# Kernel tuning notes

Hardware: AMD Instinct MI355X
Metric: run time of the kernel (lower is better)

## Reference

```python
import jax, jax.numpy as jnp
import numpy as np

S, B, D, E, H, REQ = 2048, 4, 256, 256, 8, 16  # seq, batch, hidden_dim, embed(=hidden_size), heads, band half-width


def setup_inputs() -> dict:
    key = jax.random.key(0)
    ks = jax.random.split(key, 12)
    w = lambda k, shape: jax.random.normal(k, shape, jnp.float32) * 0.02
    return {
        "mod": jax.random.normal(ks[0], (S, B, D), jnp.float32),
        "mask": jnp.zeros((B, S), jnp.float32),  # unused in speaker=False branch (kept for fidelity)
        "Wq": w(ks[1], (E, D)), "bq": jnp.zeros((E,), jnp.float32),
        "Wk": w(ks[2], (E, D)), "bk": jnp.zeros((E,), jnp.float32),
        "Wv": w(ks[3], (E, D)), "bv": jnp.zeros((E,), jnp.float32),
        "Win": w(ks[4], (3 * E, E)), "bin_": jnp.zeros((3 * E,), jnp.float32),  # MHA in_proj
        "Wout": w(ks[5], (E, E)), "bout": jnp.zeros((E,), jnp.float32),         # MHA out_proj
        "Wfc": w(ks[6], (D, E)), "bfc": jnp.zeros((D,), jnp.float32),           # self.fc
        "gamma": jnp.ones((D,), jnp.float32), "beta": jnp.zeros((D,), jnp.float32),
        "req": REQ,
    }


def reference(mod, mask, Wq, bq, Wk, bk, Wv, bv, Win, bin_, Wout, bout, Wfc, bfc, gamma, beta, req):
    s, b, d = mod.shape
    e = Wq.shape[0]
    hd = e // H
    # fc_q/k/v (pre-projection) then MultiheadAttention's own in_proj
    q = mod @ Wq.T + bq                       # (s, b, e)
    k = mod @ Wk.T + bk
    v = mod @ Wv.T + bv
    q = q @ Win[:e].T + bin_[:e]
    k = k @ Win[e:2 * e].T + bin_[e:2 * e]
    v = v @ Win[2 * e:].T + bin_[2 * e:]
    split = lambda x: x.reshape(s, b, H, hd).transpose(1, 2, 0, 3)  # (b, H, s, hd)
    qh, kh, vh = split(q), split(k), split(v)
    scores = jnp.einsum('bhqd,bhkd->bhqk', qh, kh) / jnp.sqrt(jnp.float32(hd))
    idx = jnp.arange(s)
    allowed = jnp.abs(idx[:, None] - idx[None, :]) < req  # band: diag + offsets 1..req-1
    scores = jnp.where(allowed[None, None], scores, -jnp.inf)
    attn = jax.nn.softmax(scores, axis=-1)                # attn dropout = identity (eval)
    ctx = jnp.einsum('bhqk,bhkd->bhqd', attn, vh)
    ctx = ctx.transpose(2, 0, 1, 3).reshape(s, b, e)
    ctx = ctx @ Wout.T + bout
    y = ctx @ Wfc.T + bfc + mod                           # dropout(0.5) = identity (eval), residual
    mu = jnp.mean(y, axis=-1, keepdims=True)
    var = jnp.var(y, axis=-1, keepdims=True)
    return (y - mu) / jnp.sqrt(var + 1e-6) * gamma + beta
```

## Files before the change

### kernel.cpp

```cpp
#include <hip/hip_runtime.h>
#include <hip/hip_bf16.h>
#include <math.h>

#define SS 2048
#define BB 4
#define DD 256
#define EE 256
#define HH 8
#define HD 32
#define TT (SS*BB)

typedef unsigned short ushortt;
typedef __attribute__((ext_vector_type(8))) short short8;
typedef __attribute__((ext_vector_type(4))) float f32x4;

__device__ __forceinline__ float bfbits2f(ushortt u) {
    return __uint_as_float(((unsigned int)u) << 16);
}
__device__ __forceinline__ ushortt f2bf_bits(float f) {
    unsigned int u = __float_as_uint(f);
    unsigned int r = u + 0x7FFFu + ((u >> 16) & 1u);
    return (ushortt)(r >> 16);
}

__device__ __forceinline__ int robust_req(const void* p) {
    int i = *(const int*)p;
    if (i >= 1 && i <= SS) return i;
    float f = __int_as_float(i);
    if (f >= 1.f && f <= (float)SS) return (int)(f + 0.5f);
    float b = bfbits2f(*(const ushortt*)p);
    if (b >= 1.f && b <= (float)SS) return (int)(b + 0.5f);
    return 16;
}

__global__ __launch_bounds__(256)
void fuse_fold(const float* __restrict__ mod,
               const float* __restrict__ Win,
               const float* __restrict__ Wq, const float* __restrict__ Wk,
               const float* __restrict__ Wv,
               const float* __restrict__ bq, const float* __restrict__ bk,
               const float* __restrict__ bv, const float* __restrict__ bin_,
               const float* __restrict__ Wfc, const float* __restrict__ Wout,
               const float* __restrict__ bout, const float* __restrict__ bfc,
               ushortt* __restrict__ Weffb, float* __restrict__ beff,
               ushortt* __restrict__ W2b, float* __restrict__ b2,
               ushortt* __restrict__ modb) {
    __shared__ __align__(16) ushortt ALds[64][264];
    __shared__ __align__(16) ushortt BLds[64][264];
    const int t = threadIdx.x;

    {
        size_t base = (size_t)blockIdx.x * 2048 + (size_t)t * 8;
        float4 v0 = *(const float4*)(mod + base);
        float4 v1 = *(const float4*)(mod + base + 4);
        ushort4 o0, o1;
        o0.x = f2bf_bits(v0.x); o0.y = f2bf_bits(v0.y);
        o0.z = f2bf_bits(v0.z); o0.w = f2bf_bits(v0.w);
        o1.x = f2bf_bits(v1.x); o1.y = f2bf_bits(v1.y);
        o1.z = f2bf_bits(v1.z); o1.w = f2bf_bits(v1.w);
        *(ushort4*)(modb + base)     = o0;
        *(ushort4*)(modb + base + 4) = o1;
    }
    if (blockIdx.x >= 64) return;

    const int mat = blockIdx.x >> 4;
    const int mt  = (blockIdx.x >> 2) & 3;
    const int nt  = blockIdx.x & 3;
    const int m0  = mt * 64, n0 = nt * 64;

    const float* Asrc = (mat == 3) ? (Wfc + (size_t)m0 * EE)
                                   : (Win + ((size_t)mat * EE + m0) * EE);
    const float* Bsrc = (mat == 0) ? Wq : (mat == 1) ? Wk : (mat == 2) ? Wv : Wout;

#pragma unroll
    for (int i = 0; i < 16; ++i) {
        int slot = t + 256 * i;
        int row = slot >> 6, c4 = slot & 63;
        float4 v = *(const float4*)(Asrc + (size_t)row * EE + c4 * 4);
        ushort4 o;
        o.x = f2bf_bits(v.x); o.y = f2bf_bits(v.y);
        o.z = f2bf_bits(v.z); o.w = f2bf_bits(v.w);
        *(ushort4*)&ALds[row][c4 * 4] = o;
    }
#pragma unroll
    for (int i = 0; i < 16; ++i) {
        int slot = t + 256 * i;
        int k = slot >> 4, c4 = slot & 15;
        float4 v = *(const float4*)(Bsrc + (size_t)k * DD + n0 + c4 * 4);
        BLds[c4 * 4 + 0][k] = f2bf_bits(v.x);
        BLds[c4 * 4 + 1][k] = f2bf_bits(v.y);
        BLds[c4 * 4 + 2][k] = f2bf_bits(v.z);
        BLds[c4 * 4 + 3][k] = f2bf_bits(v.w);
    }
    if (nt == 0) {
        const float* bvec = (mat == 0) ? bq : (mat == 1) ? bk : (mat == 2) ? bv : bout;
        int r = t >> 2, qq = t & 3;
        const float* arow = Asrc + (size_t)r * EE + qq * 64;
        const float* bv64 = bvec + qq * 64;
        float p = 0.f;
#pragma unroll
        for (int j = 0; j < 64; ++j) p += arow[j] * bv64[j];
        p += __shfl_xor(p, 1);
        p += __shfl_xor(p, 2);
        if (qq == 0) {
            if (mat == 3) b2[m0 + r] = p + bfc[m0 + r];
            else          beff[mat * EE + m0 + r] = p + bin_[mat * EE + m0 + r];
        }
    }
    __syncthreads();

    const int w = t >> 6, lane = t & 63, quad = lane >> 4, l16 = lane & 15;
    const int wm = w >> 1, wn = w & 1;
    f32x4 acc[2][2];
#pragma unroll
    for (int fm = 0; fm < 2; ++fm)
#pragma unroll
        for (int fn = 0; fn < 2; ++fn) acc[fm][fn] = (f32x4){0.f, 0.f, 0.f, 0.f};
#pragma unroll
    for (int kf = 0; kf < 8; ++kf) {
        short8 af0 = *(const short8*)&ALds[wm * 32 + l16][kf * 32 + quad * 8];
        short8 af1 = *(const short8*)&ALds[wm * 32 + 16 + l16][kf * 32 + quad * 8];
        short8 bf0 = *(const short8*)&BLds[wn * 32 + l16][kf * 32 + quad * 8];
        short8 bf1 = *(const short8*)&BLds[wn * 32 + 16 + l16][kf * 32 + quad * 8];
        acc[0][0] = __builtin_amdgcn_mfma_f32_16x16x32_bf16(af0, bf0, acc[0][0], 0, 0, 0);
        acc[0][1] = __builtin_amdgcn_mfma_f32_16x16x32_bf16(af0, bf1, acc[0][1], 0, 0, 0);
        acc[1][0] = __builtin_amdgcn_mfma_f32_16x16x32_bf16(af1, bf0, acc[1][0], 0, 0, 0);
        acc[1][1] = __builtin_amdgcn_mfma_f32_16x16x32_bf16(af1, bf1, acc[1][1], 0, 0, 0);
    }
    ushortt* Cd = (mat == 3) ? W2b : (Weffb + (size_t)mat * EE * DD);
#pragma unroll
    for (int fm = 0; fm < 2; ++fm)
#pragma unroll
        for (int fn = 0; fn < 2; ++fn)
#pragma unroll
            for (int r = 0; r < 4; ++r) {
                int row = m0 + wm * 32 + fm * 16 + quad * 4 + r;
                int col = n0 + wn * 32 + fn * 16 + l16;
                Cd[(size_t)row * DD + col] = f2bf_bits(acc[fm][fn][r]);
            }
}

__global__ __launch_bounds__(256)
void gemm_qkv(const ushortt* __restrict__ A, const ushortt* __restrict__ Bw,
              const float* __restrict__ bias, ushortt* __restrict__ C) {
    const int t    = threadIdx.x;
    const int lane = t & 63;
    const int w    = t >> 6;
    const int quad = lane >> 4;
    const int l16  = lane & 15;
    const int n0   = blockIdx.x * 96;
    const int m0   = blockIdx.y * 64 + w * 16;
    const int N    = 3 * EE, K = DD;

    short8 af[8];
    const ushortt* arow = A + (size_t)(m0 + l16) * K + quad * 8;
#pragma unroll
    for (int kf = 0; kf < 8; ++kf)
        af[kf] = *(const short8*)(arow + kf * 32);

    f32x4 acc[6];
#pragma unroll
    for (int fn = 0; fn < 6; ++fn) acc[fn] = (f32x4){0.f, 0.f, 0.f, 0.f};

#pragma unroll
    for (int fn = 0; fn < 6; ++fn) {
        const ushortt* brow = Bw + (size_t)(n0 + fn * 16 + l16) * K + quad * 8;
#pragma unroll
        for (int kf = 0; kf < 8; ++kf) {
            short8 bfr = *(const short8*)(brow + kf * 32);
            acc[fn] = __builtin_amdgcn_mfma_f32_16x16x32_bf16(af[kf], bfr, acc[fn], 0, 0, 0);
        }
    }

#pragma unroll
    for (int fn = 0; fn < 6; ++fn)
#pragma unroll
        for (int r = 0; r < 4; ++r) {
            int row = (m0 & ~15) + quad * 4 + r + (m0 & 15);
            row = m0 + quad * 4 + r;
            int col = n0 + fn * 16 + l16;
            C[(size_t)row * N + col] = f2bf_bits(acc[fn][r] + bias[col]);
        }
}

__global__ __launch_bounds__(256)
void attn_mfma(const ushortt* __restrict__ qkv,
               const void* __restrict__ reqp,
               ushortt* __restrict__ ctx) {
    __shared__ __align__(16) ushortt Plds[4][16 * 72];
    const int t    = threadIdx.x;
    const int w    = t >> 6;
    const int lane = t & 63;
    const int l16  = lane & 15;
    const int quad = lane >> 4;
    const int wid  = blockIdx.x * 4 + w;
    const int stile = wid >> 5;
    const int rem   = wid & 31;
    const int b = rem >> 3;
    const int h = rem & 7;
    const int s0 = stile * 16;
    const int req = robust_req(reqp);

    const ushortt* qptr = qkv + ((size_t)(s0 + l16) * BB + b) * (3 * EE) + h * HD + quad * 8;
    short8 aq = *(const short8*)qptr;

    f32x4 sc[3];
#pragma unroll
    for (int kt = 0; kt < 3; ++kt) {
        int j = s0 - 16 + kt * 16 + l16;
        int jc = min(max(j, 0), SS - 1);
        const ushortt* kp = qkv + ((size_t)jc * BB + b) * (3 * EE) + EE + h * HD + quad * 8;
        short8 bk = *(const short8*)kp;
        sc[kt] = __builtin_amdgcn_mfma_f32_16x16x32_bf16(aq, bk, (f32x4){0.f,0.f,0.f,0.f}, 0, 0, 0);
    }

    const float scale = 0.17677669529663687f;
    float pv[3][4];
#pragma unroll
    for (int r = 0; r < 4; ++r) {
        int s = s0 + quad * 4 + r;
        float vv[3];
        float mx = -INFINITY;
#pragma unroll
        for (int kt = 0; kt < 3; ++kt) {
            int j = s0 - 16 + kt * 16 + l16;
            int dj = s - j;
            bool valid = (j >= 0) && (j < SS) && (dj < req) && (-dj < req);
            vv[kt] = valid ? sc[kt][r] * scale : -INFINITY;
            mx = fmaxf(mx, vv[kt]);
        }
#pragma unroll
        for (int off = 1; off <= 8; off <<= 1) mx = fmaxf(mx, __shfl_xor(mx, off));
        float sum = 0.f;
#pragma unroll
        for (int kt = 0; kt < 3; ++kt) {
            float p = (vv[kt] > -INFINITY) ? __expf(vv[kt] - mx) : 0.f;
            pv[kt][r] = p;
            sum += p;
        }
#pragma unroll
        for (int off = 1; off <= 8; off <<= 1) sum += __shfl_xor(sum, off);
        float inv = 1.f / sum;
#pragma unroll
        for (int kt = 0; kt < 3; ++kt) pv[kt][r] *= inv;
    }

    ushortt* P = &Plds[w][0];
#pragma unroll
    for (int kt = 0; kt < 3; ++kt)
#pragma unroll
        for (int r = 0; r < 4; ++r)
            P[(quad * 4 + r) * 72 + kt * 16 + l16] = f2bf_bits(pv[kt][r]);
#pragma unroll
    for (int r = 0; r < 4; ++r)
        P[(quad * 4 + r) * 72 + 48 + l16] = 0;
    __syncthreads();

    short8 pa[2];
    pa[0] = *(const short8*)&P[l16 * 72 + quad * 8];
    pa[1] = *(const short8*)&P[l16 * 72 + 32 + quad * 8];

    f32x4 acc[2];
    acc[0] = (f32x4){0.f,0.f,0.f,0.f};
    acc[1] = (f32x4){0.f,0.f,0.f,0.f};
#pragma unroll
    for (int c = 0; c < 2; ++c) {
#pragma unroll
        for (int nd = 0; nd < 2; ++nd) {
            short8 bv;
#pragma unroll
            for (int u = 0; u < 8; ++u) {
                int j = s0 - 16 + c * 32 + quad * 8 + u;
                int jc = min(max(j, 0), SS - 1);
                bv[u] = (short)qkv[((size_t)jc * BB + b) * (3 * EE) + 2 * EE + h * HD + nd * 16 + l16];
            }
            acc[nd] = __builtin_amdgcn_mfma_f32_16x16x32_bf16(pa[c], bv, acc[nd], 0, 0, 0);
        }
    }

#pragma unroll
    for (int nd = 0; nd < 2; ++nd)
#pragma unroll
        for (int r = 0; r < 4; ++r) {
            int tok = (s0 + quad * 4 + r) * BB + b;
            ctx[(size_t)tok * EE + h * HD + nd * 16 + l16] = f2bf_bits(acc[nd][r]);
        }
}

__global__ __launch_bounds__(256)
void gemm_tail_ln(const ushortt* __restrict__ A, const ushortt* __restrict__ Bw,
                  const float* __restrict__ b2, const float* __restrict__ mod,
                  const float* __restrict__ gamma, const float* __restrict__ beta,
                  float* __restrict__ out) {
    __shared__ __align__(16) ushortt Alds[32][72];
    __shared__ __align__(16) ushortt Blds[256][72];
    __shared__ float part1[4][32], part2[4][32];
    const int t    = threadIdx.x;
    const int lane = t & 63;
    const int w    = t >> 6;
    const int quad = lane >> 4;
    const int l16  = lane & 15;
    const int m0   = blockIdx.x * 32;
    const int K    = EE;

    f32x4 acc[2][4];
#pragma unroll
    for (int fm = 0; fm < 2; ++fm)
#pragma unroll
        for (int fn = 0; fn < 4; ++fn) acc[fm][fn] = (f32x4){0.f,0.f,0.f,0.f};

    for (int k0 = 0; k0 < K; k0 += 64) {
        {
            int row = t >> 3, c8 = (t & 7) * 8;
            *(float4*)&Alds[row][c8] = *(const float4*)(A + (size_t)(m0 + row) * K + k0 + c8);
        }
#pragma unroll
        for (int i = 0; i < 8; ++i) {
            int slot = t + 256 * i;
            int row = slot >> 3, c8 = (slot & 7) * 8;
            *(float4*)&Blds[row][c8] = *(const float4*)(Bw + (size_t)row * K + k0 + c8);
        }
        __syncthreads();
        short8 af[2][2], bfr[4][2];
#pragma unroll
        for (int fm = 0; fm < 2; ++fm)
#pragma unroll
            for (int kf = 0; kf < 2; ++kf)
                af[fm][kf] = *(const short8*)&Alds[fm * 16 + l16][kf * 32 + quad * 8];
#pragma unroll
        for (int fn = 0; fn < 4; ++fn)
#pragma unroll
            for (int kf = 0; kf < 2; ++kf)
                bfr[fn][kf] = *(const short8*)&Blds[w * 64 + fn * 16 + l16][kf * 32 + quad * 8];
#pragma unroll
        for (int kf = 0; kf < 2; ++kf)
#pragma unroll
            for (int fm = 0; fm < 2; ++fm)
#pragma unroll
                for (int fn = 0; fn < 4; ++fn)
                    acc[fm][fn] = __builtin_amdgcn_mfma_f32_16x16x32_bf16(
                        af[fm][kf], bfr[fn][kf], acc[fm][fn], 0, 0, 0);
        __syncthreads();
    }

#pragma unroll
    for (int fm = 0; fm < 2; ++fm) {
#pragma unroll
        for (int r = 0; r < 4; ++r) {
            int rowl = fm * 16 + quad * 4 + r;
            int row  = m0 + rowl;
            float s1 = 0.f, s2 = 0.f;
#pragma unroll
            for (int fn = 0; fn < 4; ++fn) {
                int col = w * 64 + fn * 16 + l16;
                float v = acc[fm][fn][r] + b2[col] + mod[(size_t)row * DD + col];
                acc[fm][fn][r] = v;
                s1 += v;
                s2 += v * v;
            }
#pragma unroll
            for (int off = 1; off <= 8; off <<= 1) {
                s1 += __shfl_xor(s1, off);
                s2 += __shfl_xor(s2, off);
            }
            if (l16 == 0) { part1[w][rowl] = s1; part2[w][rowl] = s2; }
        }
    }
    __syncthreads();
#pragma unroll
    for (int fm = 0; fm < 2; ++fm) {
#pragma unroll
        for (int r = 0; r < 4; ++r) {
            int rowl = fm * 16 + quad * 4 + r;
            int row  = m0 + rowl;
            float S1 = part1[0][rowl] + part1[1][rowl] + part1[2][rowl] + part1[3][rowl];
            float S2 = part2[0][rowl] + part2[1][rowl] + part2[2][rowl] + part2[3][rowl];
            float mean = S1 * (1.f / DD);
            float var  = S2 * (1.f / DD) - mean * mean;
            float inv  = rsqrtf(var + 1e-6f);
#pragma unroll
            for (int fn = 0; fn < 4; ++fn) {
                int col = w * 64 + fn * 16 + l16;
                out[(size_t)row * DD + col] = (acc[fm][fn][r] - mean) * inv * gamma[col] + beta[col];
            }
        }
    }
}

extern "C" void kernel_launch(void* const* d_in, const int* in_sizes, int n_in,
                              void* d_out, int out_size, void* d_ws, size_t ws_size,
                              hipStream_t stream) {
    const float* mod  = (const float*)d_in[0];
    const float* Wq   = (const float*)d_in[2];
    const float* bq   = (const float*)d_in[3];
    const float* Wk   = (const float*)d_in[4];
    const float* bk   = (const float*)d_in[5];
    const float* Wv   = (const float*)d_in[6];
    const float* bv   = (const float*)d_in[7];
    const float* Win  = (const float*)d_in[8];
    const float* bin_ = (const float*)d_in[9];
    const float* Wout = (const float*)d_in[10];
    const float* bout = (const float*)d_in[11];
    const float* Wfc  = (const float*)d_in[12];
    const float* bfc  = (const float*)d_in[13];
    const float* gamma= (const float*)d_in[14];
    const float* beta = (const float*)d_in[15];
    const void*  reqp = d_in[16];

    float* out = (float*)d_out;

    float*  beff = (float*)d_ws;
    float*  b2   = beff + 3 * EE;
    ushortt* Weffb = (ushortt*)(b2 + DD);
    ushortt* W2b   = Weffb + 3 * EE * DD;
    ushortt* modb  = W2b + DD * EE;
    ushortt* qkvb  = modb + (size_t)TT * DD;
    ushortt* ctxb  = qkvb + (size_t)TT * 3 * EE;

    fuse_fold<<<1024, 256, 0, stream>>>(mod, Win, Wq, Wk, Wv, bq, bk, bv, bin_,
                                        Wfc, Wout, bout, bfc,
                                        Weffb, beff, W2b, b2, modb);
    gemm_qkv<<<dim3(8, TT / 64), 256, 0, stream>>>(modb, Weffb, beff, qkvb);
    attn_mfma<<<4096 / 4, 256, 0, stream>>>(qkvb, reqp, ctxb);
    gemm_tail_ln<<<TT / 32, 256, 0, stream>>>(ctxb, W2b, b2, mod, gamma, beta, out);
}
```

Measured before the change: 146.1 us.

## Stage QKV GEMM operands through LDS with a 2x2 warp tile layout

The QKV projection GEMM previously had each wave load its own A rows and the full 96-column B slice straight from global memory, so every wave re-read B. It now cooperatively stages 64x64 A and 96x64 B chunks into shared memory per K step, and the waves are arranged in a 2x2 grid, each computing a 32x48 output tile. This is meant to cut redundant global traffic for the weight matrix and improve reuse, at the cost of two block barriers per K iteration and no overlap between loading and compute.

Result: faster. 131.7 us (-9.9%).

```diff
diff --git a/kernel.cpp b/kernel.cpp
--- a/kernel.cpp
+++ b/kernel.cpp
@@ -143,44 +143,69 @@
 __global__ __launch_bounds__(256)
 void gemm_qkv(const ushortt* __restrict__ A, const ushortt* __restrict__ Bw,
               const float* __restrict__ bias, ushortt* __restrict__ C) {
+    __shared__ __align__(16) ushortt Alds[64][72];
+    __shared__ __align__(16) ushortt Blds[96][72];
     const int t    = threadIdx.x;
     const int lane = t & 63;
     const int w    = t >> 6;
+    const int wm   = w >> 1, wn = w & 1;
     const int quad = lane >> 4;
     const int l16  = lane & 15;
     const int n0   = blockIdx.x * 96;
-    const int m0   = blockIdx.y * 64 + w * 16;
+    const int m0   = blockIdx.y * 64;
     const int N    = 3 * EE, K = DD;
 
-    short8 af[8];
-    const ushortt* arow = A + (size_t)(m0 + l16) * K + quad * 8;
-#pragma unroll
-    for (int kf = 0; kf < 8; ++kf)
-        af[kf] = *(const short8*)(arow + kf * 32);
-
-    f32x4 acc[6];
-#pragma unroll
-    for (int fn = 0; fn < 6; ++fn) acc[fn] = (f32x4){0.f, 0.f, 0.f, 0.f};
-
-#pragma unroll
-    for (int fn = 0; fn < 6; ++fn) {
-        const ushortt* brow = Bw + (size_t)(n0 + fn * 16 + l16) * K + quad * 8;
-#pragma unroll
-        for (int kf = 0; kf < 8; ++kf) {
-            short8 bfr = *(const short8*)(brow + kf * 32);
-            acc[fn] = __builtin_amdgcn_mfma_f32_16x16x32_bf16(af[kf], bfr, acc[fn], 0, 0, 0);
-        }
-    }
-
-#pragma unroll
-    for (int fn = 0; fn < 6; ++fn)
-#pragma unroll
-        for (int r = 0; r < 4; ++r) {
-            int row = (m0 & ~15) + quad * 4 + r + (m0 & 15);
-            row = m0 + quad * 4 + r;
-            int col = n0 + fn * 16 + l16;
-            C[(size_t)row * N + col] = f2bf_bits(acc[fn][r] + bias[col]);
-        }
+    f32x4 acc[2][3];
+#pragma unroll
+    for (int fm = 0; fm < 2; ++fm)
+#pragma unroll
+        for (int fn = 0; fn < 3; ++fn) acc[fm][fn] = (f32x4){0.f,0.f,0.f,0.f};
+
+    for (int k0 = 0; k0 < K; k0 += 64) {
+        {
+            int row = t >> 2, c8 = (t & 3) * 8;
+            const ushortt* ap = A + (size_t)(m0 + row) * K + k0;
+            *(float4*)&Alds[row][c8]      = *(const float4*)(ap + c8);
+            *(float4*)&Alds[row][c8 + 32] = *(const float4*)(ap + c8 + 32);
+        }
+#pragma unroll
+        for (int i = 0; i < 3; ++i) {
+            int slot = t + 256 * i;
+            int row = slot >> 3, c8 = (slot & 7) * 8;
+            *(float4*)&Blds[row][c8] = *(const float4*)(Bw + (size_t)(n0 + row) * K + k0 + c8);
+        }
+        __syncthreads();
+        short8 af[2][2], bfr[3][2];
+#pragma unroll
+        for (int fm = 0; fm < 2; ++fm)
+#pragma unroll
+            for (int kf = 0; kf < 2; ++kf)
+                af[fm][kf] = *(const short8*)&Alds[wm * 32 + fm * 16 + l16][kf * 32 + quad * 8];
+#pragma unroll
+        for (int fn = 0; fn < 3; ++fn)
+#pragma unroll
+            for (int kf = 0; kf < 2; ++kf)
+                bfr[fn][kf] = *(const short8*)&Blds[wn * 48 + fn * 16 + l16][kf * 32 + quad * 8];
+#pragma unroll
+        for (int kf = 0; kf < 2; ++kf)
+#pragma unroll
+            for (int fm = 0; fm < 2; ++fm)
+#pragma unroll
+                for (int fn = 0; fn < 3; ++fn)
+                    acc[fm][fn] = __builtin_amdgcn_mfma_f32_16x16x32_bf16(
+                        af[fm][kf], bfr[fn][kf], acc[fm][fn], 0, 0, 0);
+        __syncthreads();
+    }
+#pragma unroll
+    for (int fm = 0; fm < 2; ++fm)
+#pragma unroll
+        for (int fn = 0; fn < 3; ++fn)
+#pragma unroll
+            for (int r = 0; r < 4; ++r) {
+                int row = m0 + wm * 32 + fm * 16 + quad * 4 + r;
+                int col = n0 + wn * 48 + fn * 16 + l16;
+                C[(size_t)row * N + col] = f2bf_bits(acc[fm][fn][r] + bias[col]);
+            }
 }
 
 __global__ __launch_bounds__(256)
```
